# Performance work log

Measured on AMD Instinct MI355X. Metric: run time of the kernel, lower is better.

## Reference

```python
import jax, jax.numpy as jnp
import numpy as np

N, C, D = 8192, 21, 5


def setup_inputs() -> dict:
    key = jax.random.key(0)
    k1, k2 = jax.random.split(key)
    U = jax.random.normal(k1, (N, C), dtype=jnp.float32)
    ref = jax.random.normal(k2, (N, D), dtype=jnp.float32)
    return {"U": U, "ref": ref}


def reference(U, ref):
    # Exact Gaussian lattice filter: out_i = sum_j exp(-||f_i - f_j||^2 / 2) U_j - U_i
    # (the permutohedral lattice is an approximation of this kernel matvec).
    sq = jnp.sum(ref * ref, axis=-1)                      # [N]
    # pairwise squared distances: ||f_i||^2 + ||f_j||^2 - 2 f_i.f_j
    d2 = sq[:, None] + sq[None, :] - 2.0 * (ref @ ref.T)  # [N, N]
    W = jnp.exp(-0.5 * jnp.maximum(d2, 0.0))              # [N, N] Gaussian kernel
    return W @ U - U                                      # (W - I) @ U
```

## Files before the change

kernel.cpp:

```cpp
#include <hip/hip_runtime.h>
#include <hip/hip_bf16.h>


#define NN 8192
#define CC 21
#define DD 5
#define NTILE_G (NN / 32)
#define ROWS 32
#define NIB (NN / ROWS)
#define JSPLIT 4
#define TPB (NTILE_G / JSPLIT)
#define BLOCK 512
#define NWAVE 8
#define TPW (TPB / NWAVE)

#define F_OFF 0
#define U_OFF (NTILE_G * 64 * 16)

typedef __attribute__((ext_vector_type(8)))  short    bf16x8;
typedef __attribute__((ext_vector_type(16))) float    f32x16;
typedef __attribute__((ext_vector_type(4)))  unsigned u32x4;

__device__ __forceinline__ short bf16s(float x) {
    __hip_bfloat16 h = __float2bfloat16(x);
    short s; __builtin_memcpy(&s, &h, 2); return s;
}
__device__ __forceinline__ float bf16f(short s) {
    __hip_bfloat16 h; __builtin_memcpy(&h, &s, 2); return __bfloat162float(h);
}

__global__ __launch_bounds__(256)
void pack_frags(const float* __restrict__ U, const float* __restrict__ ref,
                char* __restrict__ ws) {
    const float NH = -0.7213475204444817f;
    const int q = blockIdx.x * 256 + threadIdx.x;
    if (q < NTILE_G * 64) {
        const int tile = q >> 6, ln = q & 63;
        const int j = tile * 32 + (ln & 31);
        const float* fj = ref + (size_t)j * DD;
        short h_[5], l_[5];
        float sq = 0.f;
        #pragma unroll
        for (int d = 0; d < DD; ++d) {
            const float f = fj[d];
            sq = fmaf(f, f, sq);
            h_[d] = bf16s(f);
            l_[d] = bf16s(f - bf16f(h_[d]));
        }
        const float a = NH * sq;
        const short ajh = bf16s(a);
        const short ajl = bf16s(a - bf16f(ajh));
        short v[8] __attribute__((aligned(16)));
        if (ln < 32) {
            v[0]=h_[0]; v[1]=h_[1]; v[2]=h_[2]; v[3]=h_[3];
            v[4]=h_[4]; v[5]=l_[0]; v[6]=l_[1]; v[7]=l_[2];
        } else {
            v[0]=l_[3]; v[1]=l_[4]; v[2]=h_[0]; v[3]=h_[1];
            v[4]=h_[2]; v[5]=ajh;   v[6]=ajl;   v[7]=h_[3];
        }
        u32x4 pk; __builtin_memcpy(&pk, v, 16);
        *(u32x4*)(ws + F_OFF + (size_t)q * 16) = pk;
    } else {
        const int qu = q - NTILE_G * 64;
        const int ln = qu & 63, kt = (qu >> 6) & 1, tile = qu >> 7;
        const int c = ln & 31, g = ln >> 5;
        short v[8] __attribute__((aligned(16))) = {0,0,0,0,0,0,0,0};
        if (c < CC) {
            #pragma unroll
            for (int e = 0; e < 8; ++e) {
                const int j = tile * 32 + kt * 16 + (e & 3) + 8 * (e >> 2) + 4 * g;
                v[e] = bf16s(U[(size_t)j * CC + c]);
            }
        }
        u32x4 pk; __builtin_memcpy(&pk, v, 16);
        *(u32x4*)(ws + U_OFF + (size_t)qu * 16) = pk;
    }
}

__global__ __launch_bounds__(BLOCK, 8)
void lattice_main(const float* __restrict__ U, const float* __restrict__ ref,
                  const char* __restrict__ ws, float* __restrict__ out) {
    __shared__ __align__(16) float red[NWAVE * ROWS * 32];

    const int t    = threadIdx.x;
    const int lane = t & 63;
    const int wv   = t >> 6;
    const int h    = lane >> 5;
    const int m    = lane & 31;
    const int ibase = blockIdx.x * ROWS;
    const int jc    = blockIdx.y;
    const float L  = 1.4426950408889634f;
    const float NH = -0.7213475204444817f;

    const float* fiP = ref + (size_t)(ibase + m) * DD;
    const float fi0 = fiP[0], fi1 = fiP[1], fi2 = fiP[2], fi3 = fiP[3], fi4 = fiP[4];
    const float ai = NH * (fi0*fi0 + fi1*fi1 + fi2*fi2 + fi3*fi3 + fi4*fi4);
    bf16x8 bfi;
    {
        const float sf[5] = {L*fi0, L*fi1, L*fi2, L*fi3, L*fi4};
        short hi_[5], lo_[5];
        #pragma unroll
        for (int d = 0; d < DD; ++d) {
            hi_[d] = bf16s(sf[d]);
            lo_[d] = bf16s(sf[d] - bf16f(hi_[d]));
        }
        const short one = bf16s(1.0f);
        short bv[8] __attribute__((aligned(16)));
        bv[0] = h ? hi_[3] : hi_[0];
        bv[1] = h ? hi_[4] : hi_[1];
        bv[2] = h ? lo_[0] : hi_[2];
        bv[3] = h ? lo_[1] : hi_[3];
        bv[4] = h ? lo_[2] : hi_[4];
        bv[5] = h ? one    : hi_[0];
        bv[6] = h ? one    : hi_[1];
        bv[7] = h ? lo_[3] : hi_[2];
        __builtin_memcpy(&bfi, bv, 16);
    }

    f32x16 acc;
    #pragma unroll
    for (int r = 0; r < 16; ++r) acc[r] = 0.f;

    const char* Fws = ws + F_OFF;
    const char* Uws = ws + U_OFF;
    const int tile0 = jc * TPB + wv * TPW;

    for (int s = 0; s < TPW; ++s) {
        const int tile = tile0 + s;
        const u32x4 fr = *(const u32x4*)(Fws + ((size_t)(tile * 64 + lane)) * 16);
        const u32x4 b0 = *(const u32x4*)(Uws + ((size_t)((tile * 2 + 0) * 64 + lane)) * 16);
        const u32x4 b1 = *(const u32x4*)(Uws + ((size_t)((tile * 2 + 1) * 64 + lane)) * 16);

        f32x16 sacc;
        #pragma unroll
        for (int r = 0; r < 16; ++r) sacc[r] = 0.f;
        sacc = __builtin_amdgcn_mfma_f32_32x32x16_bf16(
            __builtin_bit_cast(bf16x8, fr), bfi, sacc, 0, 0, 0);

        short wv16[16] __attribute__((aligned(16)));
        #pragma unroll
        for (int r = 0; r < 16; ++r)
            wv16[r] = bf16s(__builtin_amdgcn_exp2f(ai + sacc[r]));
        bf16x8 a0, a1;
        __builtin_memcpy(&a0, &wv16[0], 16);
        __builtin_memcpy(&a1, &wv16[8], 16);

        acc = __builtin_amdgcn_mfma_f32_32x32x16_bf16(
            a0, __builtin_bit_cast(bf16x8, b0), acc, 0, 0, 0);
        acc = __builtin_amdgcn_mfma_f32_32x32x16_bf16(
            a1, __builtin_bit_cast(bf16x8, b1), acc, 0, 0, 0);
    }

    #pragma unroll
    for (int r = 0; r < 16; ++r) {
        const int row = (r & 3) + 8 * (r >> 2) + 4 * h;
        red[wv * (ROWS * 32) + row * 32 + m] = acc[r];
    }
    __syncthreads();

    #pragma unroll
    for (int k = 0; k < 2; ++k) {
        const int idx = k * BLOCK + t;
        const int row = idx >> 5, col = idx & 31;
        float s = 0.f;
        #pragma unroll
        for (int w = 0; w < NWAVE; ++w) s += red[w * (ROWS * 32) + row * 32 + col];
        if (col < CC) {
            const size_t o = (size_t)(ibase + row) * CC + col;
            if (jc == 0) s -= U[o];
            unsafeAtomicAdd(&out[o], s);
        }
    }
}

extern "C" void kernel_launch(void* const* d_in, const int* in_sizes, int n_in,
                              void* d_out, int out_size, void* d_ws, size_t ws_size,
                              hipStream_t stream) {
    const float* U   = (const float*)d_in[0];
    const float* ref = (const float*)d_in[1];
    float* out = (float*)d_out;
    char* ws = (char*)d_ws;

    hipMemsetAsync(out, 0, (size_t)out_size * sizeof(float), stream);

    const int pack_threads = NTILE_G * 64 + NTILE_G * 2 * 64;
    pack_frags<<<pack_threads / 256, 256, 0, stream>>>(U, ref, ws);

    dim3 grid(NIB, JSPLIT);
    lattice_main<<<grid, BLOCK, 0, stream>>>(U, ref, (const char*)ws, out);
}
```

Baseline: 25.05 us.

## Switch MFMA to fp16, drop j-split atomics and memset with 1024-thread blocks

Converts the operands and MFMAs from bf16 to fp16, which allows a single fp16 term for the norm instead of a hi/lo split. The column dimension is no longer split across a grid y-dimension: each block uses 16 waves covering all j tiles and reduces them in shared memory. It then writes the output directly, removing the memset and the atomics. The trade-offs are fewer, larger blocks (256 blocks of 1024 threads with 64KB of LDS) and fp16 range and precision risk for the exp weights and U values.

```diff
diff --git a/kernel.cpp b/kernel.cpp
--- a/kernel.cpp
+++ b/kernel.cpp
@@ -1,5 +1,4 @@
 #include <hip/hip_runtime.h>
-#include <hip/hip_bf16.h>
 
 
 #define NN 8192
@@ -8,26 +7,16 @@
 #define NTILE_G (NN / 32)
 #define ROWS 32
 #define NIB (NN / ROWS)
-#define JSPLIT 4
-#define TPB (NTILE_G / JSPLIT)
-#define BLOCK 512
-#define NWAVE 8
-#define TPW (TPB / NWAVE)
+#define MAINT 1024
+#define NWAVE 16
+#define TPW (NTILE_G / NWAVE)
 
 #define F_OFF 0
 #define U_OFF (NTILE_G * 64 * 16)
 
-typedef __attribute__((ext_vector_type(8)))  short    bf16x8;
+typedef __attribute__((ext_vector_type(8)))  _Float16 f16x8;
 typedef __attribute__((ext_vector_type(16))) float    f32x16;
 typedef __attribute__((ext_vector_type(4)))  unsigned u32x4;
-
-__device__ __forceinline__ short bf16s(float x) {
-    __hip_bfloat16 h = __float2bfloat16(x);
-    short s; __builtin_memcpy(&s, &h, 2); return s;
-}
-__device__ __forceinline__ float bf16f(short s) {
-    __hip_bfloat16 h; __builtin_memcpy(&h, &s, 2); return __bfloat162float(h);
-}
 
 __global__ __launch_bounds__(256)
 void pack_frags(const float* __restrict__ U, const float* __restrict__ ref,
@@ -38,25 +27,23 @@
         const int tile = q >> 6, ln = q & 63;
         const int j = tile * 32 + (ln & 31);
         const float* fj = ref + (size_t)j * DD;
-        short h_[5], l_[5];
+        _Float16 h_[5], l_[5];
         float sq = 0.f;
         #pragma unroll
         for (int d = 0; d < DD; ++d) {
             const float f = fj[d];
             sq = fmaf(f, f, sq);
-            h_[d] = bf16s(f);
-            l_[d] = bf16s(f - bf16f(h_[d]));
+            h_[d] = (_Float16)f;
+            l_[d] = (_Float16)(f - (float)h_[d]);
         }
-        const float a = NH * sq;
-        const short ajh = bf16s(a);
-        const short ajl = bf16s(a - bf16f(ajh));
-        short v[8] __attribute__((aligned(16)));
+        const _Float16 aj = (_Float16)(NH * sq);
+        _Float16 v[8] __attribute__((aligned(16)));
         if (ln < 32) {
             v[0]=h_[0]; v[1]=h_[1]; v[2]=h_[2]; v[3]=h_[3];
             v[4]=h_[4]; v[5]=l_[0]; v[6]=l_[1]; v[7]=l_[2];
         } else {
             v[0]=l_[3]; v[1]=l_[4]; v[2]=h_[0]; v[3]=h_[1];
-            v[4]=h_[2]; v[5]=ajh;   v[6]=ajl;   v[7]=h_[3];
+            v[4]=h_[2]; v[5]=h_[3]; v[6]=h_[4]; v[7]=aj;
         }
         u32x4 pk; __builtin_memcpy(&pk, v, 16);
         *(u32x4*)(ws + F_OFF + (size_t)q * 16) = pk;
@@ -64,12 +51,12 @@
         const int qu = q - NTILE_G * 64;
         const int ln = qu & 63, kt = (qu >> 6) & 1, tile = qu >> 7;
         const int c = ln & 31, g = ln >> 5;
-        short v[8] __attribute__((aligned(16))) = {0,0,0,0,0,0,0,0};
+        _Float16 v[8] __attribute__((aligned(16))) = {0,0,0,0,0,0,0,0};
         if (c < CC) {
             #pragma unroll
             for (int e = 0; e < 8; ++e) {
                 const int j = tile * 32 + kt * 16 + (e & 3) + 8 * (e >> 2) + 4 * g;
-                v[e] = bf16s(U[(size_t)j * CC + c]);
+                v[e] = (_Float16)U[(size_t)j * CC + c];
             }
         }
         u32x4 pk; __builtin_memcpy(&pk, v, 16);
@@ -77,7 +64,7 @@
     }
 }
 
-__global__ __launch_bounds__(BLOCK, 8)
+__global__ __launch_bounds__(MAINT, 4)
 void lattice_main(const float* __restrict__ U, const float* __restrict__ ref,
                   const char* __restrict__ ws, float* __restrict__ out) {
     __shared__ __align__(16) float red[NWAVE * ROWS * 32];
@@ -88,32 +75,30 @@
     const int h    = lane >> 5;
     const int m    = lane & 31;
     const int ibase = blockIdx.x * ROWS;
-    const int jc    = blockIdx.y;
     const float L  = 1.4426950408889634f;
     const float NH = -0.7213475204444817f;
 
     const float* fiP = ref + (size_t)(ibase + m) * DD;
     const float fi0 = fiP[0], fi1 = fiP[1], fi2 = fiP[2], fi3 = fiP[3], fi4 = fiP[4];
     const float ai = NH * (fi0*fi0 + fi1*fi1 + fi2*fi2 + fi3*fi3 + fi4*fi4);
-    bf16x8 bfi;
+    f16x8 bfi;
     {
         const float sf[5] = {L*fi0, L*fi1, L*fi2, L*fi3, L*fi4};
-        short hi_[5], lo_[5];
+        _Float16 hi_[5], lo_[5];
         #pragma unroll
         for (int d = 0; d < DD; ++d) {
-            hi_[d] = bf16s(sf[d]);
-            lo_[d] = bf16s(sf[d] - bf16f(hi_[d]));
+            hi_[d] = (_Float16)sf[d];
+            lo_[d] = (_Float16)(sf[d] - (float)hi_[d]);
         }
-        const short one = bf16s(1.0f);
-        short bv[8] __attribute__((aligned(16)));
+        _Float16 bv[8] __attribute__((aligned(16)));
         bv[0] = h ? hi_[3] : hi_[0];
         bv[1] = h ? hi_[4] : hi_[1];
         bv[2] = h ? lo_[0] : hi_[2];
         bv[3] = h ? lo_[1] : hi_[3];
         bv[4] = h ? lo_[2] : hi_[4];
-        bv[5] = h ? one    : hi_[0];
-        bv[6] = h ? one    : hi_[1];
-        bv[7] = h ? lo_[3] : hi_[2];
+        bv[5] = h ? lo_[3] : hi_[0];
+        bv[6] = h ? lo_[4] : hi_[1];
+        bv[7] = h ? (_Float16)1.0f : hi_[2];
         __builtin_memcpy(&bfi, bv, 16);
     }
 
@@ -123,7 +108,7 @@
 
     const char* Fws = ws + F_OFF;
     const char* Uws = ws + U_OFF;
-    const int tile0 = jc * TPB + wv * TPW;
+    const int tile0 = wv * TPW;
 
     for (int s = 0; s < TPW; ++s) {
         const int tile = tile0 + s;
@@ -134,21 +119,21 @@
         f32x16 sacc;
         #pragma unroll
         for (int r = 0; r < 16; ++r) sacc[r] = 0.f;
-        sacc = __builtin_amdgcn_mfma_f32_32x32x16_bf16(
-            __builtin_bit_cast(bf16x8, fr), bfi, sacc, 0, 0, 0);
+        sacc = __builtin_amdgcn_mfma_f32_32x32x16_f16(
+            __builtin_bit_cast(f16x8, fr), bfi, sacc, 0, 0, 0);
 
-        short wv16[16] __attribute__((aligned(16)));
+        _Float16 wv16[16] __attribute__((aligned(16)));
         #pragma unroll
         for (int r = 0; r < 16; ++r)
-            wv16[r] = bf16s(__builtin_amdgcn_exp2f(ai + sacc[r]));
-        bf16x8 a0, a1;
+            wv16[r] = (_Float16)__builtin_amdgcn_exp2f(ai + sacc[r]);
+        f16x8 a0, a1;
         __builtin_memcpy(&a0, &wv16[0], 16);
         __builtin_memcpy(&a1, &wv16[8], 16);
 
-        acc = __builtin_amdgcn_mfma_f32_32x32x16_bf16(
-            a0, __builtin_bit_cast(bf16x8, b0), acc, 0, 0, 0);
-        acc = __builtin_amdgcn_mfma_f32_32x32x16_bf16(
-            a1, __builtin_bit_cast(bf16x8, b1), acc, 0, 0, 0);
+        acc = __builtin_amdgcn_mfma_f32_32x32x16_f16(
+            a0, __builtin_bit_cast(f16x8, b0), acc, 0, 0, 0);
+        acc = __builtin_amdgcn_mfma_f32_32x32x16_f16(
+            a1, __builtin_bit_cast(f16x8, b1), acc, 0, 0, 0);
     }
 
     #pragma unroll
@@ -158,17 +143,14 @@
     }
     __syncthreads();
 
-    #pragma unroll
-    for (int k = 0; k < 2; ++k) {
-        const int idx = k * BLOCK + t;
-        const int row = idx >> 5, col = idx & 31;
+    {
+        const int row = t >> 5, col = t & 31;
         float s = 0.f;
         #pragma unroll
         for (int w = 0; w < NWAVE; ++w) s += red[w * (ROWS * 32) + row * 32 + col];
         if (col < CC) {
             const size_t o = (size_t)(ibase + row) * CC + col;
-            if (jc == 0) s -= U[o];
-            unsafeAtomicAdd(&out[o], s);
+            out[o] = s - U[o];
         }
     }
 }
@@ -181,11 +163,7 @@
     float* out = (float*)d_out;
     char* ws = (char*)d_ws;
 
-    hipMemsetAsync(out, 0, (size_t)out_size * sizeof(float), stream);
-
     const int pack_threads = NTILE_G * 64 + NTILE_G * 2 * 64;
     pack_frags<<<pack_threads / 256, 256, 0, stream>>>(U, ref, ws);
-
-    dim3 grid(NIB, JSPLIT);
-    lattice_main<<<grid, BLOCK, 0, stream>>>(U, ref, (const char*)ws, out);
+    lattice_main<<<NIB, MAINT, 0, stream>>>(U, ref, (const char*)ws, out);
 }
```

Result: faster. 22.39 us, median of 2 (-10.6%).
